# Kernel optimization log

Hardware: AMD Instinct MI355X
Metric: run time of the kernel (lower is better)

Reference implementation:

```python
import jax, jax.numpy as jnp
import numpy as np

KH = KW = 3
STRIDE = 1
PAD = 1
DIL = 1


def setup_inputs() -> dict:
    key = jax.random.key(0)
    k1, k2, k3, k4 = jax.random.split(key, 4)
    B, C, H, W = 16, 64, 64, 64
    Cout = 64
    K = KH * KW
    x = jax.random.normal(k1, (B, C, H, W), jnp.float32)
    offset = jax.random.normal(k2, (B, 2 * K, H, W), jnp.float32)
    mask = jax.random.uniform(k3, (B, K, H, W), jnp.float32)
    # uniform(-stdv, stdv) init with stdv = 1/sqrt(C*KH*KW) ~ 0.0417; scaled normal is close enough
    weight = jax.random.normal(k4, (Cout, C, KH, KW), jnp.float32) * 0.04
    bias = jnp.zeros((Cout,), jnp.float32)  # no_bias=True -> frozen zeros, still added
    return dict(input=x, offset=offset, mask=mask, weight=weight, bias=bias)


def _bilinear(img, py, px):
    # img: [C, H, W]; py, px: [K, Ho, Wo] float sampling coords
    # DCNv2 semantics: out-of-bounds corner contributions are zero.
    H, W = img.shape[1], img.shape[2]
    y0f = jnp.floor(py)
    x0f = jnp.floor(px)
    wy = py - y0f
    wx = px - x0f
    y0 = y0f.astype(jnp.int32)
    x0 = x0f.astype(jnp.int32)
    out = jnp.zeros((img.shape[0],) + py.shape, img.dtype)
    for dy in (0, 1):
        for dx in (0, 1):
            yi = y0 + dy
            xi = x0 + dx
            valid = ((yi >= 0) & (yi < H) & (xi >= 0) & (xi < W)).astype(img.dtype)
            v = img[:, jnp.clip(yi, 0, H - 1), jnp.clip(xi, 0, W - 1)]  # [C,K,Ho,Wo]
            w = (wy if dy else 1.0 - wy) * (wx if dx else 1.0 - wx)
            out = out + v * (w * valid)[None]
    return out  # [C, K, Ho, Wo]


def reference(input, offset, mask, weight, bias):
    B, C, H, W = input.shape
    Cout, _, kh, kw = weight.shape
    K = kh * kw
    Ho = (H + 2 * PAD - (DIL * (kh - 1) + 1)) // STRIDE + 1
    Wo = (W + 2 * PAD - (DIL * (kw - 1) + 1)) // STRIDE + 1
    off = offset.reshape(B, K, 2, Ho, Wo)  # per kernel point: (dy, dx)
    ky = jnp.repeat(jnp.arange(kh), kw)  # [K] kernel row index
    kx = jnp.tile(jnp.arange(kw), kh)    # [K] kernel col index
    base_y = jnp.arange(Ho) * STRIDE - PAD
    base_x = jnp.arange(Wo) * STRIDE - PAD
    py = off[:, :, 0] + (base_y[None, None, :, None] + (ky * DIL)[None, :, None, None])
    px = off[:, :, 1] + (base_x[None, None, None, :] + (kx * DIL)[None, :, None, None])
    sampled = jax.vmap(_bilinear)(input, py, px)        # [B, C, K, Ho, Wo]
    modulated = sampled * mask[:, None]                 # mask-modulated accumulation
    out = jnp.einsum('bckpq,ock->bopq', modulated, weight.reshape(Cout, C, K))
    return out + bias[None, :, None, None]
```

## Files before the change

### kernel.cpp

```cpp
#include <hip/hip_runtime.h>
#include <hip/hip_fp16.h>

#define BATCH 16
#define C_IN  64
#define HH    64
#define WW    64
#define COUT  64
#define KK    9
#define HW    4096
#define CK    576
#define WROWS 13
#define WLO   5

typedef _Float16 f16x8 __attribute__((ext_vector_type(8)));
typedef float    f32x4 __attribute__((ext_vector_type(4)));

__device__ __forceinline__ unsigned short f32_to_f16u(float f) {
    _Float16 h = (_Float16)f;
    unsigned short u;
    __builtin_memcpy(&u, &h, 2);
    return u;
}

__device__ __forceinline__ __half2 as_h2(unsigned int u) {
    __half2 r; __builtin_memcpy(&r, &u, 4); return r;
}
__device__ __forceinline__ unsigned int as_u32(__half2 v) {
    unsigned int u; __builtin_memcpy(&u, &v, 4); return u;
}

__global__ __launch_bounds__(256) void prep_kernel(
    const float* __restrict__ x, const float* __restrict__ w,
    unsigned short* __restrict__ xt, unsigned short* __restrict__ wt) {
    __shared__ unsigned short tile[64][72];
    const int t = threadIdx.x;
    const int blk = blockIdx.x;
    if (blk < 1024) {
        const int b = blk >> 6, y = blk & 63;
        const float* xrow = x + ((b * 64) * 64 + y) * 64;
#pragma unroll
        for (int it = 0; it < 4; ++it) {
            const int idx = it * 256 + t;
            const int c = idx >> 4, seg = idx & 15;
            const float4 v = *(const float4*)(xrow + c * HW + seg * 4);
            tile[seg * 4 + 0][c] = f32_to_f16u(v.x);
            tile[seg * 4 + 1][c] = f32_to_f16u(v.y);
            tile[seg * 4 + 2][c] = f32_to_f16u(v.z);
            tile[seg * 4 + 3][c] = f32_to_f16u(v.w);
        }
        __syncthreads();
#pragma unroll
        for (int it = 0; it < 2; ++it) {
            const int idx = it * 256 + t;
            const int xx = idx >> 3, cs = idx & 7;
            *(int4*)&xt[((b * HW) + y * 64 + xx) * 64 + cs * 8] =
                *(const int4*)&tile[xx][cs * 8];
        }
    } else {
        const int i = (blk - 1024) * 256 + t;
        const int j = i & 7;
        const int l = (i >> 3) & 63;
        const int ot = (i >> 9) & 3;
        const int r = i >> 11;
        const int ks = r % 6, kc = r / 6;
        const int o  = ot * 16 + (l & 15);
        const int kk = ks * 32 + (l >> 4) * 8 + j;
        const int tap = kk >> 6, c = kk & 63;
        const int k = kc * 3 + tap;
        wt[i] = f32_to_f16u(w[o * CK + c * KK + k]);
    }
}

__global__ __launch_bounds__(512, 1) void dcn_main_kernel(
    const float* __restrict__ offset, const float* __restrict__ mask,
    const unsigned short* __restrict__ xt, const unsigned short* __restrict__ wt,
    const float* __restrict__ bias, float* __restrict__ out) {
    __shared__ __align__(16) unsigned short win[WROWS * 4096];
    __shared__ __align__(16) int PWw[2][576 * 4];
    __shared__ __align__(16) unsigned int PWa[2][576 * 4];

    const int t    = threadIdx.x;
    const int wave = __builtin_amdgcn_readfirstlane(t >> 6);
    const int lane = t & 63;
    const int quad = lane >> 4, m16 = lane & 15;
    const int rw   = wave >> 2;
    const int qb   = (wave & 3) * 16;

    const int blk = blockIdx.x;
    const int xcd = blk & 7;
    const int i6  = blk >> 3;
    const int b   = (xcd << 1) | (i6 >> 5);
    const int R   = (i6 & 31) * 2;
    const int base = R - WLO;

    const float* offb = offset + b * (2 * KK * HW);
    const float* mb   = mask + b * (KK * HW);
    const char* xtb   = (const char*)(xt + b * (HW * 64));

    float oyv[3], oxv[3], mkv[3];
#pragma unroll
    for (int p = 0; p < 3; ++p) {
        const int it = p * 512 + t;
        if (it < 1152) {
            const int rsel = it >= 576;
            const int j = it - rsel * 576;
            const int tap = j >> 6, q = j & 63;
            const int rowX = R + rsel;
            oyv[p] = offb[(2 * tap) * HW + rowX * 64 + q];
            oxv[p] = offb[(2 * tap + 1) * HW + rowX * 64 + q];
            mkv[p] = mb[tap * HW + rowX * 64 + q];
        } else { oyv[p] = 0.f; oxv[p] = 0.f; mkv[p] = 0.f; }
    }
    asm volatile("" :: "v"(oyv[0]), "v"(oxv[0]), "v"(mkv[0]),
                       "v"(oyv[1]), "v"(oxv[1]), "v"(mkv[1]),
                       "v"(oyv[2]), "v"(oxv[2]), "v"(mkv[2]));

    const int pxl = t >> 3;
    const int swb = ((t & 7) ^ (pxl & 7)) << 4;
#pragma unroll
    for (int s = 0; s < WROWS; ++s) {
        const int srcrow = min(max(base + s, 0), HH - 1);
        const char* src = xtb + srcrow * 8192 + pxl * 128 + swb;
        __builtin_amdgcn_global_load_lds(
            (const __attribute__((address_space(1))) unsigned int*)src,
            (__attribute__((address_space(3))) unsigned int*)
                ((char*)win + s * 8192 + t * 16),
            16, 0, 0);
    }
    __builtin_amdgcn_sched_barrier(0);

#pragma unroll
    for (int p = 0; p < 3; ++p) {
        const int it = p * 512 + t;
        if (it < 1152) {
            const int rsel = it >= 576;
            const int j = it - rsel * 576;
            const int tap = j >> 6, q = j & 63;
            const int rowX = R + rsel;
            const int ky = (tap * 11) >> 5;
            const int kx = tap - ky * 3;
            const float py  = oyv[p] + (float)(rowX - 1 + ky);
            const float pxf = oxv[p] + (float)(q - 1 + kx);
            const float y0f = floorf(py), x0f = floorf(pxf);
            const float wy = py - y0f, wx = pxf - x0f;
            const int y0 = (int)y0f, x0 = (int)x0f;
            const int y1 = y0 + 1,   x1 = x0 + 1;
            const float vy0 = (y0 >= 0 && y0 < HH) ? 1.f : 0.f;
            const float vy1 = (y1 >= 0 && y1 < HH) ? 1.f : 0.f;
            const float vx0 = (x0 >= 0 && x0 < WW) ? 1.f : 0.f;
            const float vx1 = (x1 >= 0 && x1 < WW) ? 1.f : 0.f;
            const float mk = mkv[p];
            const float w00 = (1.f - wy) * (1.f - wx) * vy0 * vx0 * mk;
            const float w01 = (1.f - wy) * wx         * vy0 * vx1 * mk;
            const float w10 = wy * (1.f - wx)         * vy1 * vx0 * mk;
            const float w11 = wy * wx                 * vy1 * vx1 * mk;
            const int cy0 = min(max(y0, 0), HH - 1), cy1 = min(max(y1, 0), HH - 1);
            const int cx0 = min(max(x0, 0), WW - 1), cx1 = min(max(x1, 0), WW - 1);
            const int sl0 = cy0 - base, sl1 = cy1 - base;
            const unsigned esc = (sl0 < 0) | (sl1 > (WROWS - 1));
            const int c0 = min(max(sl0, 0), WROWS - 1);
            const int c1 = min(max(sl1, 0), WROWS - 1);
            const int wl00 = c0 * 64 + cx0, wl01 = c0 * 64 + cx1;
            const int wl10 = c1 * 64 + cx0, wl11 = c1 * 64 + cx1;
            const unsigned int s00 = f32_to_f16u(w00);
            const unsigned int s01 = f32_to_f16u(w01);
            const unsigned int s10 = f32_to_f16u(w10);
            const unsigned int s11 = f32_to_f16u(w11);
            int4 P0;
            P0.x = (int)(s00 | (s00 << 16));
            P0.y = (int)(s01 | (s01 << 16));
            P0.z = (int)(s10 | (s10 << 16));
            P0.w = (int)(s11 | (s11 << 16));
            *(int4*)&PWw[rsel][j * 4] = P0;
            uint4 A;
            A.x = (unsigned)((wl00 << 7) | ((wl00 & 7) << 4)) | (esc << 31);
            A.y = (unsigned)((wl01 << 7) | ((wl01 & 7) << 4));
            A.z = (unsigned)((wl10 << 7) | ((wl10 & 7) << 4));
            A.w = (unsigned)((wl11 << 7) | ((wl11 & 7) << 4));
            *(uint4*)&PWa[rsel][j * 4] = A;
        }
    }
    __syncthreads();

    f32x4 acc[4];
#pragma unroll
    for (int ot = 0; ot < 4; ++ot)
#pragma unroll
        for (int r = 0; r < 4; ++r) acc[ot][r] = 0.f;

    const char* winc = (const char*)win;
    const int rowX = R + rw;

#pragma unroll
    for (int kc = 0; kc < 3; ++kc) {
        const unsigned short* wkc = wt + kc * (6 * 4 * 512);
#pragma unroll
        for (int ks = 0; ks < 6; ++ks) {
            const int tap = kc * 3 + (ks >> 1);
            const int it  = tap * 64 + qb + m16;
            const uint4 A  = *(const uint4*)&PWa[rw][it * 4];
            const int4  p0 = *(const int4*)&PWw[rw][it * 4];
            const unsigned sswz = (unsigned)(((ks & 1) * 4 + quad) << 4);
            uint4 q0 = *(const uint4*)(winc + ((A.x & 0x7FFFFFFFu) ^ sswz));
            uint4 q1 = *(const uint4*)(winc + (A.y ^ sswz));
            uint4 q2 = *(const uint4*)(winc + (A.z ^ sswz));
            uint4 q3 = *(const uint4*)(winc + (A.w ^ sswz));
            if (__builtin_expect(__any((int)(A.x >> 31)), 0)) {
                if (A.x >> 31) {
                    const int q = qb + m16;
                    const int ky = (tap * 11) >> 5;
                    const int kx = tap - ky * 3;
                    const float oy = offb[(2 * tap) * HW + rowX * 64 + q];
                    const float ox = offb[(2 * tap + 1) * HW + rowX * 64 + q];
                    const float py  = oy + (float)(rowX - 1 + ky);
                    const float pxf = ox + (float)(q - 1 + kx);
                    const int y0 = (int)floorf(py), x0 = (int)floorf(pxf);
                    const int cy0 = min(max(y0, 0), HH - 1);
                    const int cy1 = min(max(y0 + 1, 0), HH - 1);
                    const int cx0 = min(max(x0, 0), WW - 1);
                    const int cx1 = min(max(x0 + 1, 0), WW - 1);
                    const int hoff = (ks & 1) * 64 + quad * 16;
                    q0 = *(const uint4*)(xtb + ((cy0 * 64 + cx0) << 7) + hoff);
                    q1 = *(const uint4*)(xtb + ((cy0 * 64 + cx1) << 7) + hoff);
                    q2 = *(const uint4*)(xtb + ((cy1 * 64 + cx0) << 7) + hoff);
                    q3 = *(const uint4*)(xtb + ((cy1 * 64 + cx1) << 7) + hoff);
                }
            }
            const __half2 c00 = as_h2((unsigned)p0.x);
            const __half2 c01 = as_h2((unsigned)p0.y);
            const __half2 c10 = as_h2((unsigned)p0.z);
            const __half2 c11 = as_h2((unsigned)p0.w);
            uint4 ov;
            {
                __half2 v = __hmul2(c00, as_h2(q0.x));
                v = __hfma2(c01, as_h2(q1.x), v);
                v = __hfma2(c10, as_h2(q2.x), v);
                v = __hfma2(c11, as_h2(q3.x), v);
                ov.x = as_u32(v);
            }
            {
                __half2 v = __hmul2(c00, as_h2(q0.y));
                v = __hfma2(c01, as_h2(q1.y), v);
                v = __hfma2(c10, as_h2(q2.y), v);
                v = __hfma2(c11, as_h2(q3.y), v);
                ov.y = as_u32(v);
            }
            {
                __half2 v = __hmul2(c00, as_h2(q0.z));
                v = __hfma2(c01, as_h2(q1.z), v);
                v = __hfma2(c10, as_h2(q2.z), v);
                v = __hfma2(c11, as_h2(q3.z), v);
                ov.z = as_u32(v);
            }
            {
                __half2 v = __hmul2(c00, as_h2(q0.w));
                v = __hfma2(c01, as_h2(q1.w), v);
                v = __hfma2(c10, as_h2(q2.w), v);
                v = __hfma2(c11, as_h2(q3.w), v);
                ov.w = as_u32(v);
            }
            f16x8 bfrag;
            __builtin_memcpy(&bfrag, &ov, 16);
#pragma unroll
            for (int ot = 0; ot < 4; ++ot) {
                const f16x8 afrag =
                    *(const f16x8*)(wkc + (ks * 4 + ot) * 512 + lane * 8);
                acc[ot] = __builtin_amdgcn_mfma_f32_16x16x32_f16(afrag, bfrag,
                                                                 acc[ot], 0, 0, 0);
            }
        }
    }

    float* ob = out + b * (COUT * HW) + rowX * 64 + qb + m16;
#pragma unroll
    for (int ot = 0; ot < 4; ++ot)
#pragma unroll
        for (int r = 0; r < 4; ++r) {
            const int o = ot * 16 + quad * 4 + r;
            ob[o * HW] = acc[ot][r] + bias[o];
        }
}

extern "C" void kernel_launch(void* const* d_in, const int* in_sizes, int n_in,
                              void* d_out, int out_size, void* d_ws,
                              size_t ws_size, hipStream_t stream) {
    const float* x    = (const float*)d_in[0];
    const float* off  = (const float*)d_in[1];
    const float* mask = (const float*)d_in[2];
    const float* w    = (const float*)d_in[3];
    const float* bias = (const float*)d_in[4];
    float* out = (float*)d_out;

    unsigned short* xt = (unsigned short*)d_ws;
    unsigned short* wt = (unsigned short*)((char*)d_ws + 8388608);

    prep_kernel<<<1024 + 144, 256, 0, stream>>>(x, w, xt, wt);
    dcn_main_kernel<<<512, 512, 0, stream>>>(off, mask, xt, wt, bias, out);
}
```

Before: 96.92 us.

## Process four output rows per block with a taller LDS window, simplify prep transpose

```diff
diff --git a/kernel.cpp b/kernel.cpp
--- a/kernel.cpp
+++ b/kernel.cpp
@@ -9,7 +9,7 @@
 #define KK    9
 #define HW    4096
 #define CK    576
-#define WROWS 13
+#define WROWS 15
 #define WLO   5
 
 typedef _Float16 f16x8 __attribute__((ext_vector_type(8)));
@@ -32,30 +32,22 @@
 __global__ __launch_bounds__(256) void prep_kernel(
     const float* __restrict__ x, const float* __restrict__ w,
     unsigned short* __restrict__ xt, unsigned short* __restrict__ wt) {
-    __shared__ unsigned short tile[64][72];
     const int t = threadIdx.x;
     const int blk = blockIdx.x;
     if (blk < 1024) {
         const int b = blk >> 6, y = blk & 63;
-        const float* xrow = x + ((b * 64) * 64 + y) * 64;
-#pragma unroll
-        for (int it = 0; it < 4; ++it) {
-            const int idx = it * 256 + t;
-            const int c = idx >> 4, seg = idx & 15;
-            const float4 v = *(const float4*)(xrow + c * HW + seg * 4);
-            tile[seg * 4 + 0][c] = f32_to_f16u(v.x);
-            tile[seg * 4 + 1][c] = f32_to_f16u(v.y);
-            tile[seg * 4 + 2][c] = f32_to_f16u(v.z);
-            tile[seg * 4 + 3][c] = f32_to_f16u(v.w);
+        const int px = t & 63, cg = t >> 6;
+        const float* xp = x + ((b * 64 + cg * 16) * 64 + y) * 64 + px;
+        unsigned int u[8];
+#pragma unroll
+        for (int j = 0; j < 8; ++j) {
+            const float v0 = xp[(2 * j) * HW];
+            const float v1 = xp[(2 * j + 1) * HW];
+            u[j] = (unsigned)f32_to_f16u(v0) | ((unsigned)f32_to_f16u(v1) << 16);
         }
-        __syncthreads();
-#pragma unroll
-        for (int it = 0; it < 2; ++it) {
-            const int idx = it * 256 + t;
-            const int xx = idx >> 3, cs = idx & 7;
-            *(int4*)&xt[((b * HW) + y * 64 + xx) * 64 + cs * 8] =
-                *(const int4*)&tile[xx][cs * 8];
-        }
+        unsigned short* dst = xt + ((b * HW) + y * 64 + px) * 64 + cg * 16;
+        *(uint4*)dst = *(const uint4*)&u[0];
+        *(uint4*)(dst + 8) = *(const uint4*)&u[4];
     } else {
         const int i = (blk - 1024) * 256 + t;
         const int j = i & 7;
@@ -88,32 +80,37 @@
 
     const int blk = blockIdx.x;
     const int xcd = blk & 7;
-    const int i6  = blk >> 3;
-    const int b   = (xcd << 1) | (i6 >> 5);
-    const int R   = (i6 & 31) * 2;
-    const int base = R - WLO;
+    const int i5  = blk >> 3;
+    const int b   = (xcd << 1) | (i5 >> 4);
+    const int R4  = (i5 & 15) * 4;
+    const int base = R4 - WLO;
 
     const float* offb = offset + b * (2 * KK * HW);
     const float* mb   = mask + b * (KK * HW);
     const char* xtb   = (const char*)(xt + b * (HW * 64));
 
-    float oyv[3], oxv[3], mkv[3];
-#pragma unroll
-    for (int p = 0; p < 3; ++p) {
-        const int it = p * 512 + t;
-        if (it < 1152) {
-            const int rsel = it >= 576;
-            const int j = it - rsel * 576;
-            const int tap = j >> 6, q = j & 63;
-            const int rowX = R + rsel;
-            oyv[p] = offb[(2 * tap) * HW + rowX * 64 + q];
-            oxv[p] = offb[(2 * tap + 1) * HW + rowX * 64 + q];
-            mkv[p] = mb[tap * HW + rowX * 64 + q];
-        } else { oyv[p] = 0.f; oxv[p] = 0.f; mkv[p] = 0.f; }
-    }
-    asm volatile("" :: "v"(oyv[0]), "v"(oxv[0]), "v"(mkv[0]),
-                       "v"(oyv[1]), "v"(oxv[1]), "v"(mkv[1]),
-                       "v"(oyv[2]), "v"(oxv[2]), "v"(mkv[2]));
+    float oyv[2][3], oxv[2][3], mkv[2][3];
+#pragma unroll
+    for (int pr = 0; pr < 2; ++pr)
+#pragma unroll
+        for (int p = 0; p < 3; ++p) {
+            const int it = p * 512 + t;
+            if (it < 1152) {
+                const int rsel = it >= 576;
+                const int j = it - rsel * 576;
+                const int tap = j >> 6, q = j & 63;
+                const int rowX = R4 + pr * 2 + rsel;
+                oyv[pr][p] = offb[(2 * tap) * HW + rowX * 64 + q];
+                oxv[pr][p] = offb[(2 * tap + 1) * HW + rowX * 64 + q];
+                mkv[pr][p] = mb[tap * HW + rowX * 64 + q];
+            } else { oyv[pr][p] = 0.f; oxv[pr][p] = 0.f; mkv[pr][p] = 0.f; }
+        }
+    asm volatile("" :: "v"(oyv[0][0]), "v"(oxv[0][0]), "v"(mkv[0][0]),
+                       "v"(oyv[0][1]), "v"(oxv[0][1]), "v"(mkv[0][1]),
+                       "v"(oyv[0][2]), "v"(oxv[0][2]), "v"(mkv[0][2]));
+    asm volatile("" :: "v"(oyv[1][0]), "v"(oxv[1][0]), "v"(mkv[1][0]),
+                       "v"(oyv[1][1]), "v"(oxv[1][1]), "v"(mkv[1][1]),
+                       "v"(oyv[1][2]), "v"(oxv[1][2]), "v"(mkv[1][2]));
 
     const int pxl = t >> 3;
     const int swb = ((t & 7) ^ (pxl & 7)) << 4;
@@ -129,156 +126,169 @@
     }
     __builtin_amdgcn_sched_barrier(0);
 
-#pragma unroll
-    for (int p = 0; p < 3; ++p) {
-        const int it = p * 512 + t;
-        if (it < 1152) {
-            const int rsel = it >= 576;
-            const int j = it - rsel * 576;
-            const int tap = j >> 6, q = j & 63;
-            const int rowX = R + rsel;
-            const int ky = (tap * 11) >> 5;
-            const int kx = tap - ky * 3;
-            const float py  = oyv[p] + (float)(rowX - 1 + ky);
-            const float pxf = oxv[p] + (float)(q - 1 + kx);
-            const float y0f = floorf(py), x0f = floorf(pxf);
-            const float wy = py - y0f, wx = pxf - x0f;
-            const int y0 = (int)y0f, x0 = (int)x0f;
-            const int y1 = y0 + 1,   x1 = x0 + 1;
-            const float vy0 = (y0 >= 0 && y0 < HH) ? 1.f : 0.f;
-            const float vy1 = (y1 >= 0 && y1 < HH) ? 1.f : 0.f;
-            const float vx0 = (x0 >= 0 && x0 < WW) ? 1.f : 0.f;
-            const float vx1 = (x1 >= 0 && x1 < WW) ? 1.f : 0.f;
-            const float mk = mkv[p];
-            const float w00 = (1.f - wy) * (1.f - wx) * vy0 * vx0 * mk;
-            const float w01 = (1.f - wy) * wx         * vy0 * vx1 * mk;
-            const float w10 = wy * (1.f - wx)         * vy1 * vx0 * mk;
-            const float w11 = wy * wx                 * vy1 * vx1 * mk;
-            const int cy0 = min(max(y0, 0), HH - 1), cy1 = min(max(y1, 0), HH - 1);
-            const int cx0 = min(max(x0, 0), WW - 1), cx1 = min(max(x1, 0), WW - 1);
-            const int sl0 = cy0 - base, sl1 = cy1 - base;
-            const unsigned esc = (sl0 < 0) | (sl1 > (WROWS - 1));
-            const int c0 = min(max(sl0, 0), WROWS - 1);
-            const int c1 = min(max(sl1, 0), WROWS - 1);
-            const int wl00 = c0 * 64 + cx0, wl01 = c0 * 64 + cx1;
-            const int wl10 = c1 * 64 + cx0, wl11 = c1 * 64 + cx1;
-            const unsigned int s00 = f32_to_f16u(w00);
-            const unsigned int s01 = f32_to_f16u(w01);
-            const unsigned int s10 = f32_to_f16u(w10);
-            const unsigned int s11 = f32_to_f16u(w11);
-            int4 P0;
-            P0.x = (int)(s00 | (s00 << 16));
-            P0.y = (int)(s01 | (s01 << 16));
-            P0.z = (int)(s10 | (s10 << 16));
-            P0.w = (int)(s11 | (s11 << 16));
-            *(int4*)&PWw[rsel][j * 4] = P0;
-            uint4 A;
-            A.x = (unsigned)((wl00 << 7) | ((wl00 & 7) << 4)) | (esc << 31);
-            A.y = (unsigned)((wl01 << 7) | ((wl01 & 7) << 4));
-            A.z = (unsigned)((wl10 << 7) | ((wl10 & 7) << 4));
-            A.w = (unsigned)((wl11 << 7) | ((wl11 & 7) << 4));
-            *(uint4*)&PWa[rsel][j * 4] = A;
-        }
-    }
-    __syncthreads();
-
-    f32x4 acc[4];
-#pragma unroll
-    for (int ot = 0; ot < 4; ++ot)
-#pragma unroll
-        for (int r = 0; r < 4; ++r) acc[ot][r] = 0.f;
-
-    const char* winc = (const char*)win;
-    const int rowX = R + rw;
-
-#pragma unroll
-    for (int kc = 0; kc < 3; ++kc) {
-        const unsigned short* wkc = wt + kc * (6 * 4 * 512);
-#pragma unroll
-        for (int ks = 0; ks < 6; ++ks) {
-            const int tap = kc * 3 + (ks >> 1);
-            const int it  = tap * 64 + qb + m16;
-            const uint4 A  = *(const uint4*)&PWa[rw][it * 4];
-            const int4  p0 = *(const int4*)&PWw[rw][it * 4];
-            const unsigned sswz = (unsigned)(((ks & 1) * 4 + quad) << 4);
-            uint4 q0 = *(const uint4*)(winc + ((A.x & 0x7FFFFFFFu) ^ sswz));
-            uint4 q1 = *(const uint4*)(winc + (A.y ^ sswz));
-            uint4 q2 = *(const uint4*)(winc + (A.z ^ sswz));
-            uint4 q3 = *(const uint4*)(winc + (A.w ^ sswz));
-            if (__builtin_expect(__any((int)(A.x >> 31)), 0)) {
-                if (A.x >> 31) {
-                    const int q = qb + m16;
-                    const int ky = (tap * 11) >> 5;
-                    const int kx = tap - ky * 3;
-                    const float oy = offb[(2 * tap) * HW + rowX * 64 + q];
-                    const float ox = offb[(2 * tap + 1) * HW + rowX * 64 + q];
-                    const float py  = oy + (float)(rowX - 1 + ky);
-                    const float pxf = ox + (float)(q - 1 + kx);
-                    const int y0 = (int)floorf(py), x0 = (int)floorf(pxf);
-                    const int cy0 = min(max(y0, 0), HH - 1);
-                    const int cy1 = min(max(y0 + 1, 0), HH - 1);
-                    const int cx0 = min(max(x0, 0), WW - 1);
-                    const int cx1 = min(max(x0 + 1, 0), WW - 1);
-                    const int hoff = (ks & 1) * 64 + quad * 16;
-                    q0 = *(const uint4*)(xtb + ((cy0 * 64 + cx0) << 7) + hoff);
-                    q1 = *(const uint4*)(xtb + ((cy0 * 64 + cx1) << 7) + hoff);
-                    q2 = *(const uint4*)(xtb + ((cy1 * 64 + cx0) << 7) + hoff);
-                    q3 = *(const uint4*)(xtb + ((cy1 * 64 + cx1) << 7) + hoff);
-                }
-            }
-            const __half2 c00 = as_h2((unsigned)p0.x);
-            const __half2 c01 = as_h2((unsigned)p0.y);
-            const __half2 c10 = as_h2((unsigned)p0.z);
-            const __half2 c11 = as_h2((unsigned)p0.w);
-            uint4 ov;
-            {
-                __half2 v = __hmul2(c00, as_h2(q0.x));
-                v = __hfma2(c01, as_h2(q1.x), v);
-                v = __hfma2(c10, as_h2(q2.x), v);
-                v = __hfma2(c11, as_h2(q3.x), v);
-                ov.x = as_u32(v);
-            }
-            {
-                __half2 v = __hmul2(c00, as_h2(q0.y));
-                v = __hfma2(c01, as_h2(q1.y), v);
-                v = __hfma2(c10, as_h2(q2.y), v);
-                v = __hfma2(c11, as_h2(q3.y), v);
-                ov.y = as_u32(v);
-            }
-            {
-                __half2 v = __hmul2(c00, as_h2(q0.z));
-                v = __hfma2(c01, as_h2(q1.z), v);
-                v = __hfma2(c10, as_h2(q2.z), v);
-                v = __hfma2(c11, as_h2(q3.z), v);
-                ov.z = as_u32(v);
-            }
-            {
-                __half2 v = __hmul2(c00, as_h2(q0.w));
-                v = __hfma2(c01, as_h2(q1.w), v);
-                v = __hfma2(c10, as_h2(q2.w), v);
-                v = __hfma2(c11, as_h2(q3.w), v);
-                ov.w = as_u32(v);
-            }
-            f16x8 bfrag;
-            __builtin_memcpy(&bfrag, &ov, 16);
-#pragma unroll
-            for (int ot = 0; ot < 4; ++ot) {
-                const f16x8 afrag =
-                    *(const f16x8*)(wkc + (ks * 4 + ot) * 512 + lane * 8);
-                acc[ot] = __builtin_amdgcn_mfma_f32_16x16x32_f16(afrag, bfrag,
-                                                                 acc[ot], 0, 0, 0);
+    auto computePW = [&](int pr) {
+#pragma unroll
+        for (int p = 0; p < 3; ++p) {
+            const int it = p * 512 + t;
+            if (it < 1152) {
+                const int rsel = it >= 576;
+                const int j = it - rsel * 576;
+                const int tap = j >> 6, q = j & 63;
+                const int rowX = R4 + pr * 2 + rsel;
+                const int ky = (tap * 11) >> 5;
+                const int kx = tap - ky * 3;
+                const float py  = oyv[pr][p] + (float)(rowX - 1 + ky);
+                const float pxf = oxv[pr][p] + (float)(q - 1 + kx);
+                const float y0f = floorf(py), x0f = floorf(pxf);
+                const float wy = py - y0f, wx = pxf - x0f;
+                const int y0 = (int)y0f, x0 = (int)x0f;
+                const int y1 = y0 + 1,   x1 = x0 + 1;
+                const float vy0 = (y0 >= 0 && y0 < HH) ? 1.f : 0.f;
+                const float vy1 = (y1 >= 0 && y1 < HH) ? 1.f : 0.f;
+                const float vx0 = (x0 >= 0 && x0 < WW) ? 1.f : 0.f;
+                const float vx1 = (x1 >= 0 && x1 < WW) ? 1.f : 0.f;
+                const float mk = mkv[pr][p];
+                const float w00 = (1.f - wy) * (1.f - wx) * vy0 * vx0 * mk;
+                const float w01 = (1.f - wy) * wx         * vy0 * vx1 * mk;
+                const float w10 = wy * (1.f - wx)         * vy1 * vx0 * mk;
+                const float w11 = wy * wx                 * vy1 * vx1 * mk;
+                const int cy0 = min(max(y0, 0), HH - 1);
+                const int cy1 = min(max(y1, 0), HH - 1);
+                const int cx0 = min(max(x0, 0), WW - 1);
+                const int cx1 = min(max(x1, 0), WW - 1);
+                const int sl0 = cy0 - base, sl1 = cy1 - base;
+                const unsigned esc = (sl0 < 0) | (sl1 > (WROWS - 1));
+                const int c0 = min(max(sl0, 0), WROWS - 1);
+                const int c1 = min(max(sl1, 0), WROWS - 1);
+                const int wl00 = c0 * 64 + cx0, wl01 = c0 * 64 + cx1;
+                const int wl10 = c1 * 64 + cx0, wl11 = c1 * 64 + cx1;
+                const unsigned int s00 = f32_to_f16u(w00);
+                const unsigned int s01 = f32_to_f16u(w01);
+                const unsigned int s10 = f32_to_f16u(w10);
+                const unsigned int s11 = f32_to_f16u(w11);
+                int4 P0;
+                P0.x = (int)(s00 | (s00 << 16));
+                P0.y = (int)(s01 | (s01 << 16));
+                P0.z = (int)(s10 | (s10 << 16));
+                P0.w = (int)(s11 | (s11 << 16));
+                *(int4*)&PWw[rsel][j * 4] = P0;
+                uint4 A;
+                A.x = (unsigned)((wl00 << 7) | ((wl00 & 7) << 4)) | (esc << 31);
+                A.y = (unsigned)((wl01 << 7) | ((wl01 & 7) << 4));
+                A.z = (unsigned)((wl10 << 7) | ((wl10 & 7) << 4));
+                A.w = (unsigned)((wl11 << 7) | ((wl11 & 7) << 4));
+                *(uint4*)&PWa[rsel][j * 4] = A;
             }
         }
-    }
-
-    float* ob = out + b * (COUT * HW) + rowX * 64 + qb + m16;
-#pragma unroll
-    for (int ot = 0; ot < 4; ++ot)
-#pragma unroll
-        for (int r = 0; r < 4; ++r) {
-            const int o = ot * 16 + quad * 4 + r;
-            ob[o * HW] = acc[ot][r] + bias[o];
+    };
+
+    const char* winc = (const char*)win;
+
+    auto computePair = [&](int pr) {
+        f32x4 acc[4];
+#pragma unroll
+        for (int ot = 0; ot < 4; ++ot)
+#pragma unroll
+            for (int r = 0; r < 4; ++r) acc[ot][r] = 0.f;
+
+        const int rowX = R4 + pr * 2 + rw;
+#pragma unroll
+        for (int kc = 0; kc < 3; ++kc) {
+            const unsigned short* wkc = wt + kc * (6 * 4 * 512);
+#pragma unroll
+            for (int ks = 0; ks < 6; ++ks) {
+                const int tap = kc * 3 + (ks >> 1);
+                const int it  = tap * 64 + qb + m16;
+                const uint4 A  = *(const uint4*)&PWa[rw][it * 4];
+                const int4  p0 = *(const int4*)&PWw[rw][it * 4];
+                const unsigned sswz = (unsigned)(((ks & 1) * 4 + quad) << 4);
+                uint4 q0 = *(const uint4*)(winc + ((A.x & 0x7FFFFFFFu) ^ sswz));
+                uint4 q1 = *(const uint4*)(winc + (A.y ^ sswz));
+                uint4 q2 = *(const uint4*)(winc + (A.z ^ sswz));
+                uint4 q3 = *(const uint4*)(winc + (A.w ^ sswz));
+                if (__builtin_expect(__any((int)(A.x >> 31)), 0)) {
+                    if (A.x >> 31) {
+                        const int q = qb + m16;
+                        const int ky = (tap * 11) >> 5;
+                        const int kx = tap - ky * 3;
+                        const float oy = offb[(2 * tap) * HW + rowX * 64 + q];
+                        const float ox = offb[(2 * tap + 1) * HW + rowX * 64 + q];
+                        const float py  = oy + (float)(rowX - 1 + ky);
+                        const float pxf = ox + (float)(q - 1 + kx);
+                        const int y0 = (int)floorf(py), x0 = (int)floorf(pxf);
+                        const int cy0 = min(max(y0, 0), HH - 1);
+                        const int cy1 = min(max(y0 + 1, 0), HH - 1);
+                        const int cx0 = min(max(x0, 0), WW - 1);
+                        const int cx1 = min(max(x0 + 1, 0), WW - 1);
+                        const int hoff = (ks & 1) * 64 + quad * 16;
+                        q0 = *(const uint4*)(xtb + ((cy0 * 64 + cx0) << 7) + hoff);
+                        q1 = *(const uint4*)(xtb + ((cy0 * 64 + cx1) << 7) + hoff);
+                        q2 = *(const uint4*)(xtb + ((cy1 * 64 + cx0) << 7) + hoff);
+                        q3 = *(const uint4*)(xtb + ((cy1 * 64 + cx1) << 7) + hoff);
+                    }
+                }
+                const __half2 c00 = as_h2((unsigned)p0.x);
+                const __half2 c01 = as_h2((unsigned)p0.y);
+                const __half2 c10 = as_h2((unsigned)p0.z);
+                const __half2 c11 = as_h2((unsigned)p0.w);
+                uint4 ov;
+                {
+                    __half2 v = __hmul2(c00, as_h2(q0.x));
+                    v = __hfma2(c01, as_h2(q1.x), v);
+                    v = __hfma2(c10, as_h2(q2.x), v);
+                    v = __hfma2(c11, as_h2(q3.x), v);
+                    ov.x = as_u32(v);
+                }
+                {
+                    __half2 v = __hmul2(c00, as_h2(q0.y));
+                    v = __hfma2(c01, as_h2(q1.y), v);
+                    v = __hfma2(c10, as_h2(q2.y), v);
+                    v = __hfma2(c11, as_h2(q3.y), v);
+                    ov.y = as_u32(v);
+                }
+                {
+                    __half2 v = __hmul2(c00, as_h2(q0.z));
+                    v = __hfma2(c01, as_h2(q1.z), v);
+                    v = __hfma2(c10, as_h2(q2.z), v);
+                    v = __hfma2(c11, as_h2(q3.z), v);
+                    ov.z = as_u32(v);
+                }
+                {
+                    __half2 v = __hmul2(c00, as_h2(q0.w));
+                    v = __hfma2(c01, as_h2(q1.w), v);
+                    v = __hfma2(c10, as_h2(q2.w), v);
+                    v = __hfma2(c11, as_h2(q3.w), v);
+                    ov.w = as_u32(v);
+                }
+                f16x8 bfrag;
+                __builtin_memcpy(&bfrag, &ov, 16);
+#pragma unroll
+                for (int ot = 0; ot < 4; ++ot) {
+                    const f16x8 afrag =
+                        *(const f16x8*)(wkc + (ks * 4 + ot) * 512 + lane * 8);
+                    acc[ot] = __builtin_amdgcn_mfma_f32_16x16x32_f16(
+                        afrag, bfrag, acc[ot], 0, 0, 0);
+                }
+            }
         }
+
+        float* ob = out + b * (COUT * HW) + rowX * 64 + qb + m16;
+#pragma unroll
+        for (int ot = 0; ot < 4; ++ot)
+#pragma unroll
+            for (int r = 0; r < 4; ++r) {
+                const int o = ot * 16 + quad * 4 + r;
+                ob[o * HW] = acc[ot][r] + bias[o];
+            }
+    };
+
+    computePW(0);
+    __syncthreads();
+    computePair(0);
+    __syncthreads();
+    computePW(1);
+    __syncthreads();
+    computePair(1);
 }
 
 extern "C" void kernel_launch(void* const* d_in, const int* in_sizes, int n_in,
@@ -295,5 +305,5 @@
     unsigned short* wt = (unsigned short*)((char*)d_ws + 8388608);
 
     prep_kernel<<<1024 + 144, 256, 0, stream>>>(x, w, xt, wt);
-    dcn_main_kernel<<<512, 512, 0, stream>>>(off, mask, xt, wt, bias, out);
-}
+    dcn_main_kernel<<<256, 512, 0, stream>>>(off, mask, xt, wt, bias, out);
+}
```

After: 99.07 us. 1.02x slower.

## Process four rows per block with a ring-buffered LDS window

Applied to the files above, without the earlier changes.

```diff
diff --git a/kernel.cpp b/kernel.cpp
--- a/kernel.cpp
+++ b/kernel.cpp
@@ -88,197 +88,223 @@
 
     const int blk = blockIdx.x;
     const int xcd = blk & 7;
-    const int i6  = blk >> 3;
-    const int b   = (xcd << 1) | (i6 >> 5);
-    const int R   = (i6 & 31) * 2;
-    const int base = R - WLO;
+    const int i5  = blk >> 3;
+    const int b   = (xcd << 1) | (i5 >> 4);
+    const int R4  = (i5 & 15) * 4;
+    const int base = R4 - WLO;
 
     const float* offb = offset + b * (2 * KK * HW);
     const float* mb   = mask + b * (KK * HW);
     const char* xtb   = (const char*)(xt + b * (HW * 64));
-
-    float oyv[3], oxv[3], mkv[3];
-#pragma unroll
-    for (int p = 0; p < 3; ++p) {
-        const int it = p * 512 + t;
-        if (it < 1152) {
-            const int rsel = it >= 576;
-            const int j = it - rsel * 576;
-            const int tap = j >> 6, q = j & 63;
-            const int rowX = R + rsel;
-            oyv[p] = offb[(2 * tap) * HW + rowX * 64 + q];
-            oxv[p] = offb[(2 * tap + 1) * HW + rowX * 64 + q];
-            mkv[p] = mb[tap * HW + rowX * 64 + q];
-        } else { oyv[p] = 0.f; oxv[p] = 0.f; mkv[p] = 0.f; }
-    }
-    asm volatile("" :: "v"(oyv[0]), "v"(oxv[0]), "v"(mkv[0]),
-                       "v"(oyv[1]), "v"(oxv[1]), "v"(mkv[1]),
-                       "v"(oyv[2]), "v"(oxv[2]), "v"(mkv[2]));
+    const char* winc  = (const char*)win;
 
     const int pxl = t >> 3;
     const int swb = ((t & 7) ^ (pxl & 7)) << 4;
-#pragma unroll
-    for (int s = 0; s < WROWS; ++s) {
-        const int srcrow = min(max(base + s, 0), HH - 1);
-        const char* src = xtb + srcrow * 8192 + pxl * 128 + swb;
-        __builtin_amdgcn_global_load_lds(
-            (const __attribute__((address_space(1))) unsigned int*)src,
-            (__attribute__((address_space(3))) unsigned int*)
-                ((char*)win + s * 8192 + t * 16),
-            16, 0, 0);
+
+#pragma unroll 1
+    for (int po = 0; po < 2; ++po) {
+        const int R = R4 + 2 * po;
+
+        float oyv[3], oxv[3], mkv[3];
+#pragma unroll
+        for (int p = 0; p < 3; ++p) {
+            const int it = p * 512 + t;
+            if (it < 1152) {
+                const int rsel = it >= 576;
+                const int j = it - rsel * 576;
+                const int tap = j >> 6, q = j & 63;
+                const int rowX = R + rsel;
+                oyv[p] = offb[(2 * tap) * HW + rowX * 64 + q];
+                oxv[p] = offb[(2 * tap + 1) * HW + rowX * 64 + q];
+                mkv[p] = mb[tap * HW + rowX * 64 + q];
+            } else { oyv[p] = 0.f; oxv[p] = 0.f; mkv[p] = 0.f; }
+        }
+        asm volatile("" :: "v"(oyv[0]), "v"(oxv[0]), "v"(mkv[0]),
+                           "v"(oyv[1]), "v"(oxv[1]), "v"(mkv[1]),
+                           "v"(oyv[2]), "v"(oxv[2]), "v"(mkv[2]));
+
+        if (po) __syncthreads();
+
+        if (po == 0) {
+#pragma unroll
+            for (int s = 0; s < WROWS; ++s) {
+                const int srcrow = min(max(base + s, 0), HH - 1);
+                const char* src = xtb + srcrow * 8192 + pxl * 128 + swb;
+                __builtin_amdgcn_global_load_lds(
+                    (const __attribute__((address_space(1))) unsigned int*)src,
+                    (__attribute__((address_space(3))) unsigned int*)
+                        ((char*)win + s * 8192 + t * 16),
+                    16, 0, 0);
+            }
+        } else {
+#pragma unroll
+            for (int s2 = 0; s2 < 2; ++s2) {
+                const int srcrow = min(R4 + 8 + s2, HH - 1);
+                const char* src = xtb + srcrow * 8192 + pxl * 128 + swb;
+                __builtin_amdgcn_global_load_lds(
+                    (const __attribute__((address_space(1))) unsigned int*)src,
+                    (__attribute__((address_space(3))) unsigned int*)
+                        ((char*)win + s2 * 8192 + t * 16),
+                    16, 0, 0);
+            }
+        }
+        __builtin_amdgcn_sched_barrier(0);
+
+        const int lo = 2 * po, hi = 12 + 2 * po;
+#pragma unroll
+        for (int p = 0; p < 3; ++p) {
+            const int it = p * 512 + t;
+            if (it < 1152) {
+                const int rsel = it >= 576;
+                const int j = it - rsel * 576;
+                const int tap = j >> 6, q = j & 63;
+                const int rowX = R + rsel;
+                const int ky = (tap * 11) >> 5;
+                const int kx = tap - ky * 3;
+                const float py  = oyv[p] + (float)(rowX - 1 + ky);
+                const float pxf = oxv[p] + (float)(q - 1 + kx);
+                const float y0f = floorf(py), x0f = floorf(pxf);
+                const float wy = py - y0f, wx = pxf - x0f;
+                const int y0 = (int)y0f, x0 = (int)x0f;
+                const int y1 = y0 + 1,   x1 = x0 + 1;
+                const float vy0 = (y0 >= 0 && y0 < HH) ? 1.f : 0.f;
+                const float vy1 = (y1 >= 0 && y1 < HH) ? 1.f : 0.f;
+                const float vx0 = (x0 >= 0 && x0 < WW) ? 1.f : 0.f;
+                const float vx1 = (x1 >= 0 && x1 < WW) ? 1.f : 0.f;
+                const float mk = mkv[p];
+                const float w00 = (1.f - wy) * (1.f - wx) * vy0 * vx0 * mk;
+                const float w01 = (1.f - wy) * wx         * vy0 * vx1 * mk;
+                const float w10 = wy * (1.f - wx)         * vy1 * vx0 * mk;
+                const float w11 = wy * wx                 * vy1 * vx1 * mk;
+                const int cy0 = min(max(y0, 0), HH - 1);
+                const int cy1 = min(max(y1, 0), HH - 1);
+                const int cx0 = min(max(x0, 0), WW - 1);
+                const int cx1 = min(max(x1, 0), WW - 1);
+                const int sl0 = cy0 - base, sl1 = cy1 - base;
+                const unsigned esc = (sl0 < lo) | (sl1 > hi);
+                int c0 = min(max(sl0, lo), hi);
+                int c1 = min(max(sl1, lo), hi);
+                if (c0 >= WROWS) c0 -= WROWS;
+                if (c1 >= WROWS) c1 -= WROWS;
+                const int wl00 = c0 * 64 + cx0, wl01 = c0 * 64 + cx1;
+                const int wl10 = c1 * 64 + cx0, wl11 = c1 * 64 + cx1;
+                const unsigned int s00 = f32_to_f16u(w00);
+                const unsigned int s01 = f32_to_f16u(w01);
+                const unsigned int s10 = f32_to_f16u(w10);
+                const unsigned int s11 = f32_to_f16u(w11);
+                int4 P0;
+                P0.x = (int)(s00 | (s00 << 16));
+                P0.y = (int)(s01 | (s01 << 16));
+                P0.z = (int)(s10 | (s10 << 16));
+                P0.w = (int)(s11 | (s11 << 16));
+                *(int4*)&PWw[rsel][j * 4] = P0;
+                uint4 A;
+                A.x = (unsigned)((wl00 << 7) | ((wl00 & 7) << 4)) | (esc << 31);
+                A.y = (unsigned)((wl01 << 7) | ((wl01 & 7) << 4));
+                A.z = (unsigned)((wl10 << 7) | ((wl10 & 7) << 4));
+                A.w = (unsigned)((wl11 << 7) | ((wl11 & 7) << 4));
+                *(uint4*)&PWa[rsel][j * 4] = A;
+            }
+        }
+        __syncthreads();
+
+        f32x4 acc[4];
+#pragma unroll
+        for (int ot = 0; ot < 4; ++ot)
+#pragma unroll
+            for (int r = 0; r < 4; ++r) acc[ot][r] = 0.f;
+
+        const int rowX = R + rw;
+
+#pragma unroll
+        for (int kc = 0; kc < 3; ++kc) {
+            const unsigned short* wkc = wt + kc * (6 * 4 * 512);
+#pragma unroll
+            for (int ks = 0; ks < 6; ++ks) {
+                const int tap = kc * 3 + (ks >> 1);
+                const int it  = tap * 64 + qb + m16;
+                const uint4 A  = *(const uint4*)&PWa[rw][it * 4];
+                const int4  p0 = *(const int4*)&PWw[rw][it * 4];
+                const unsigned sswz = (unsigned)(((ks & 1) * 4 + quad) << 4);
+                uint4 q0 = *(const uint4*)(winc + ((A.x & 0x7FFFFFFFu) ^ sswz));
+                uint4 q1 = *(const uint4*)(winc + (A.y ^ sswz));
+                uint4 q2 = *(const uint4*)(winc + (A.z ^ sswz));
+                uint4 q3 = *(const uint4*)(winc + (A.w ^ sswz));
+                if (__builtin_expect(__any((int)(A.x >> 31)), 0)) {
+                    if (A.x >> 31) {
+                        const int q = qb + m16;
+                        const int ky = (tap * 11) >> 5;
+                        const int kx = tap - ky * 3;
+                        const float oy = offb[(2 * tap) * HW + rowX * 64 + q];
+                        const float ox = offb[(2 * tap + 1) * HW + rowX * 64 + q];
+                        const float py  = oy + (float)(rowX - 1 + ky);
+                        const float pxf = ox + (float)(q - 1 + kx);
+                        const int y0 = (int)floorf(py), x0 = (int)floorf(pxf);
+                        const int cy0 = min(max(y0, 0), HH - 1);
+                        const int cy1 = min(max(y0 + 1, 0), HH - 1);
+                        const int cx0 = min(max(x0, 0), WW - 1);
+                        const int cx1 = min(max(x0 + 1, 0), WW - 1);
+                        const int hoff = (ks & 1) * 64 + quad * 16;
+                        q0 = *(const uint4*)(xtb + ((cy0 * 64 + cx0) << 7) + hoff);
+                        q1 = *(const uint4*)(xtb + ((cy0 * 64 + cx1) << 7) + hoff);
+                        q2 = *(const uint4*)(xtb + ((cy1 * 64 + cx0) << 7) + hoff);
+                        q3 = *(const uint4*)(xtb + ((cy1 * 64 + cx1) << 7) + hoff);
+                    }
+                }
+                const __half2 c00 = as_h2((unsigned)p0.x);
+                const __half2 c01 = as_h2((unsigned)p0.y);
+                const __half2 c10 = as_h2((unsigned)p0.z);
+                const __half2 c11 = as_h2((unsigned)p0.w);
+                uint4 ov;
+                {
+                    __half2 v = __hmul2(c00, as_h2(q0.x));
+                    v = __hfma2(c01, as_h2(q1.x), v);
+                    v = __hfma2(c10, as_h2(q2.x), v);
+                    v = __hfma2(c11, as_h2(q3.x), v);
+                    ov.x = as_u32(v);
+                }
+                {
+                    __half2 v = __hmul2(c00, as_h2(q0.y));
+                    v = __hfma2(c01, as_h2(q1.y), v);
+                    v = __hfma2(c10, as_h2(q2.y), v);
+                    v = __hfma2(c11, as_h2(q3.y), v);
+                    ov.y = as_u32(v);
+                }
+                {
+                    __half2 v = __hmul2(c00, as_h2(q0.z));
+                    v = __hfma2(c01, as_h2(q1.z), v);
+                    v = __hfma2(c10, as_h2(q2.z), v);
+                    v = __hfma2(c11, as_h2(q3.z), v);
+                    ov.z = as_u32(v);
+                }
+                {
+                    __half2 v = __hmul2(c00, as_h2(q0.w));
+                    v = __hfma2(c01, as_h2(q1.w), v);
+                    v = __hfma2(c10, as_h2(q2.w), v);
+                    v = __hfma2(c11, as_h2(q3.w), v);
+                    ov.w = as_u32(v);
+                }
+                f16x8 bfrag;
+                __builtin_memcpy(&bfrag, &ov, 16);
+#pragma unroll
+                for (int ot = 0; ot < 4; ++ot) {
+                    const f16x8 afrag =
+                        *(const f16x8*)(wkc + (ks * 4 + ot) * 512 + lane * 8);
+                    acc[ot] = __builtin_amdgcn_mfma_f32_16x16x32_f16(
+                        afrag, bfrag, acc[ot], 0, 0, 0);
+                }
+            }
+        }
+
+        float* ob = out + b * (COUT * HW) + rowX * 64 + qb + m16;
+#pragma unroll
+        for (int ot = 0; ot < 4; ++ot)
+#pragma unroll
+            for (int r = 0; r < 4; ++r) {
+                const int o = ot * 16 + quad * 4 + r;
+                ob[o * HW] = acc[ot][r] + bias[o];
+            }
     }
-    __builtin_amdgcn_sched_barrier(0);
-
-#pragma unroll
-    for (int p = 0; p < 3; ++p) {
-        const int it = p * 512 + t;
-        if (it < 1152) {
-            const int rsel = it >= 576;
-            const int j = it - rsel * 576;
-            const int tap = j >> 6, q = j & 63;
-            const int rowX = R + rsel;
-            const int ky = (tap * 11) >> 5;
-            const int kx = tap - ky * 3;
-            const float py  = oyv[p] + (float)(rowX - 1 + ky);
-            const float pxf = oxv[p] + (float)(q - 1 + kx);
-            const float y0f = floorf(py), x0f = floorf(pxf);
-            const float wy = py - y0f, wx = pxf - x0f;
-            const int y0 = (int)y0f, x0 = (int)x0f;
-            const int y1 = y0 + 1,   x1 = x0 + 1;
-            const float vy0 = (y0 >= 0 && y0 < HH) ? 1.f : 0.f;
-            const float vy1 = (y1 >= 0 && y1 < HH) ? 1.f : 0.f;
-            const float vx0 = (x0 >= 0 && x0 < WW) ? 1.f : 0.f;
-            const float vx1 = (x1 >= 0 && x1 < WW) ? 1.f : 0.f;
-            const float mk = mkv[p];
-            const float w00 = (1.f - wy) * (1.f - wx) * vy0 * vx0 * mk;
-            const float w01 = (1.f - wy) * wx         * vy0 * vx1 * mk;
-            const float w10 = wy * (1.f - wx)         * vy1 * vx0 * mk;
-            const float w11 = wy * wx                 * vy1 * vx1 * mk;
-            const int cy0 = min(max(y0, 0), HH - 1), cy1 = min(max(y1, 0), HH - 1);
-            const int cx0 = min(max(x0, 0), WW - 1), cx1 = min(max(x1, 0), WW - 1);
-            const int sl0 = cy0 - base, sl1 = cy1 - base;
-            const unsigned esc = (sl0 < 0) | (sl1 > (WROWS - 1));
-            const int c0 = min(max(sl0, 0), WROWS - 1);
-            const int c1 = min(max(sl1, 0), WROWS - 1);
-            const int wl00 = c0 * 64 + cx0, wl01 = c0 * 64 + cx1;
-            const int wl10 = c1 * 64 + cx0, wl11 = c1 * 64 + cx1;
-            const unsigned int s00 = f32_to_f16u(w00);
-            const unsigned int s01 = f32_to_f16u(w01);
-            const unsigned int s10 = f32_to_f16u(w10);
-            const unsigned int s11 = f32_to_f16u(w11);
-            int4 P0;
-            P0.x = (int)(s00 | (s00 << 16));
-            P0.y = (int)(s01 | (s01 << 16));
-            P0.z = (int)(s10 | (s10 << 16));
-            P0.w = (int)(s11 | (s11 << 16));
-            *(int4*)&PWw[rsel][j * 4] = P0;
-            uint4 A;
-            A.x = (unsigned)((wl00 << 7) | ((wl00 & 7) << 4)) | (esc << 31);
-            A.y = (unsigned)((wl01 << 7) | ((wl01 & 7) << 4));
-            A.z = (unsigned)((wl10 << 7) | ((wl10 & 7) << 4));
-            A.w = (unsigned)((wl11 << 7) | ((wl11 & 7) << 4));
-            *(uint4*)&PWa[rsel][j * 4] = A;
-        }
-    }
-    __syncthreads();
-
-    f32x4 acc[4];
-#pragma unroll
-    for (int ot = 0; ot < 4; ++ot)
-#pragma unroll
-        for (int r = 0; r < 4; ++r) acc[ot][r] = 0.f;
-
-    const char* winc = (const char*)win;
-    const int rowX = R + rw;
-
-#pragma unroll
-    for (int kc = 0; kc < 3; ++kc) {
-        const unsigned short* wkc = wt + kc * (6 * 4 * 512);
-#pragma unroll
-        for (int ks = 0; ks < 6; ++ks) {
-            const int tap = kc * 3 + (ks >> 1);
-            const int it  = tap * 64 + qb + m16;
-            const uint4 A  = *(const uint4*)&PWa[rw][it * 4];
-            const int4  p0 = *(const int4*)&PWw[rw][it * 4];
-            const unsigned sswz = (unsigned)(((ks & 1) * 4 + quad) << 4);
-            uint4 q0 = *(const uint4*)(winc + ((A.x & 0x7FFFFFFFu) ^ sswz));
-            uint4 q1 = *(const uint4*)(winc + (A.y ^ sswz));
-            uint4 q2 = *(const uint4*)(winc + (A.z ^ sswz));
-            uint4 q3 = *(const uint4*)(winc + (A.w ^ sswz));
-            if (__builtin_expect(__any((int)(A.x >> 31)), 0)) {
-                if (A.x >> 31) {
-                    const int q = qb + m16;
-                    const int ky = (tap * 11) >> 5;
-                    const int kx = tap - ky * 3;
-                    const float oy = offb[(2 * tap) * HW + rowX * 64 + q];
-                    const float ox = offb[(2 * tap + 1) * HW + rowX * 64 + q];
-                    const float py  = oy + (float)(rowX - 1 + ky);
-                    const float pxf = ox + (float)(q - 1 + kx);
-                    const int y0 = (int)floorf(py), x0 = (int)floorf(pxf);
-                    const int cy0 = min(max(y0, 0), HH - 1);
-                    const int cy1 = min(max(y0 + 1, 0), HH - 1);
-                    const int cx0 = min(max(x0, 0), WW - 1);
-                    const int cx1 = min(max(x0 + 1, 0), WW - 1);
-                    const int hoff = (ks & 1) * 64 + quad * 16;
-                    q0 = *(const uint4*)(xtb + ((cy0 * 64 + cx0) << 7) + hoff);
-                    q1 = *(const uint4*)(xtb + ((cy0 * 64 + cx1) << 7) + hoff);
-                    q2 = *(const uint4*)(xtb + ((cy1 * 64 + cx0) << 7) + hoff);
-                    q3 = *(const uint4*)(xtb + ((cy1 * 64 + cx1) << 7) + hoff);
-                }
-            }
-            const __half2 c00 = as_h2((unsigned)p0.x);
-            const __half2 c01 = as_h2((unsigned)p0.y);
-            const __half2 c10 = as_h2((unsigned)p0.z);
-            const __half2 c11 = as_h2((unsigned)p0.w);
-            uint4 ov;
-            {
-                __half2 v = __hmul2(c00, as_h2(q0.x));
-                v = __hfma2(c01, as_h2(q1.x), v);
-                v = __hfma2(c10, as_h2(q2.x), v);
-                v = __hfma2(c11, as_h2(q3.x), v);
-                ov.x = as_u32(v);
-            }
-            {
-                __half2 v = __hmul2(c00, as_h2(q0.y));
-                v = __hfma2(c01, as_h2(q1.y), v);
-                v = __hfma2(c10, as_h2(q2.y), v);
-                v = __hfma2(c11, as_h2(q3.y), v);
-                ov.y = as_u32(v);
-            }
-            {
-                __half2 v = __hmul2(c00, as_h2(q0.z));
-                v = __hfma2(c01, as_h2(q1.z), v);
-                v = __hfma2(c10, as_h2(q2.z), v);
-                v = __hfma2(c11, as_h2(q3.z), v);
-                ov.z = as_u32(v);
-            }
-            {
-                __half2 v = __hmul2(c00, as_h2(q0.w));
-                v = __hfma2(c01, as_h2(q1.w), v);
-                v = __hfma2(c10, as_h2(q2.w), v);
-                v = __hfma2(c11, as_h2(q3.w), v);
-                ov.w = as_u32(v);
-            }
-            f16x8 bfrag;
-            __builtin_memcpy(&bfrag, &ov, 16);
-#pragma unroll
-            for (int ot = 0; ot < 4; ++ot) {
-                const f16x8 afrag =
-                    *(const f16x8*)(wkc + (ks * 4 + ot) * 512 + lane * 8);
-                acc[ot] = __builtin_amdgcn_mfma_f32_16x16x32_f16(afrag, bfrag,
-                                                                 acc[ot], 0, 0, 0);
-            }
-        }
-    }
-
-    float* ob = out + b * (COUT * HW) + rowX * 64 + qb + m16;
-#pragma unroll
-    for (int ot = 0; ot < 4; ++ot)
-#pragma unroll
-        for (int r = 0; r < 4; ++r) {
-            const int o = ot * 16 + quad * 4 + r;
-            ob[o * HW] = acc[ot][r] + bias[o];
-        }
 }
 
 extern "C" void kernel_launch(void* const* d_in, const int* in_sizes, int n_in,
@@ -295,5 +321,5 @@
     unsigned short* wt = (unsigned short*)((char*)d_ws + 8388608);
 
     prep_kernel<<<1024 + 144, 256, 0, stream>>>(x, w, xt, wt);
-    dcn_main_kernel<<<512, 512, 0, stream>>>(off, mask, xt, wt, bias, out);
-}
+    dcn_main_kernel<<<256, 512, 0, stream>>>(off, mask, xt, wt, bias, out);
+}
```

New measurement: 116.1 us. +19.8%, slower.
